# Performance work log

Measured on AMD Instinct MI355X. Metric: run time of the kernel, lower is better.

## Reference

```python
import jax, jax.numpy as jnp
import numpy as np

N_NODES = 100000
EPS = 1e-5


def _layernorm(h, gamma, beta):
    mu = jnp.mean(h, axis=-1, keepdims=True)
    var = jnp.mean(jnp.square(h - mu), axis=-1, keepdims=True)
    return (h - mu) * jax.lax.rsqrt(var + EPS) * gamma + beta


def _gcn_conv(x, W, b, row, col, inv_sqrt_deg):
    # PyG GCNConv: y = D^{-1/2} (A + I) D^{-1/2} (x W) + b, self-loops already in row/col
    xw = x @ W                                  # [N, C]
    norm = inv_sqrt_deg[row] * inv_sqrt_deg[col]  # [E+N]
    msg = xw[row] * norm[:, None]               # [E+N, C] gather
    agg = jax.ops.segment_sum(msg, col, num_segments=N_NODES)  # scatter-add
    return agg + b


def setup_inputs() -> dict:
    key = jax.random.key(0)
    ks = jax.random.split(key, 8)
    C = 256
    x = jax.random.normal(ks[0], (N_NODES, C), dtype=jnp.float32)
    all_edges = jax.random.randint(ks[1], (2, 1600000), 0, N_NODES, dtype=jnp.int32)
    s = 1.0 / np.sqrt(C)
    W1 = jax.random.uniform(ks[2], (C, C), jnp.float32, -s, s)
    b1 = jnp.zeros((C,), jnp.float32)
    W2 = jax.random.uniform(ks[3], (C, C), jnp.float32, -s, s)
    b2 = jnp.zeros((C,), jnp.float32)
    gamma = jnp.ones((C,), jnp.float32)
    beta = jnp.zeros((C,), jnp.float32)
    return {"x": x, "all_edges": all_edges, "W1": W1, "b1": b1,
            "W2": W2, "b2": b2, "gamma": gamma, "beta": beta}


def reference(x, all_edges, W1, b1, W2, b2, gamma, beta):
    # add self-loops
    loops = jnp.arange(N_NODES, dtype=all_edges.dtype)
    row = jnp.concatenate([all_edges[0], loops])
    col = jnp.concatenate([all_edges[1], loops])
    deg = jax.ops.segment_sum(jnp.ones_like(col, dtype=x.dtype), col,
                              num_segments=N_NODES)
    inv_sqrt_deg = jnp.where(deg > 0, jax.lax.rsqrt(deg), 0.0)

    z1 = jax.nn.relu(_layernorm(_gcn_conv(x, W1, b1, row, col, inv_sqrt_deg), gamma, beta))
    z2 = jax.nn.relu(_layernorm(_gcn_conv(z1, W2, b2, row, col, inv_sqrt_deg), gamma, beta))
    return (z1, z2)
```

## Files before the change

kernel.cpp:

```cpp
#include <hip/hip_runtime.h>
#include <cstdint>

#define C_DIM 256
#define EPS 1e-5f

typedef __attribute__((ext_vector_type(8))) short short8;
typedef __attribute__((ext_vector_type(4))) float f32x4;

__device__ __forceinline__ ushort f2bf(float f) {
  uint32_t u = __float_as_uint(f);
  u = (u + 0x7fffu + ((u >> 16) & 1u)) >> 16;
  return (ushort)u;
}
__device__ __forceinline__ float bflo(uint32_t p) { return __uint_as_float(p << 16); }
__device__ __forceinline__ float bfhi(uint32_t p) { return __uint_as_float(p & 0xffff0000u); }

__global__ void k_count(const int* __restrict__ col, int E, int* cnt) {
  int e = blockIdx.x * blockDim.x + threadIdx.x;
  if (e < E) atomicAdd(&cnt[col[e]], 1);
}

__global__ void k_isd(int* cnt, float* isd, int n) {
  int i = blockIdx.x * blockDim.x + threadIdx.x;
  if (i < n) { isd[i] = rsqrtf((float)(cnt[i] + 1)); cnt[i] = 0; }
}

__global__ void k_scan1(const int* __restrict__ cnt, int* excl, int* bsum, int n) {
  __shared__ int s[1024];
  int i = blockIdx.x * 1024 + threadIdx.x;
  int v = (i < n) ? cnt[i] : 0;
  s[threadIdx.x] = v;
  __syncthreads();
  for (int off = 1; off < 1024; off <<= 1) {
    int t = (threadIdx.x >= off) ? s[threadIdx.x - off] : 0;
    __syncthreads();
    s[threadIdx.x] += t;
    __syncthreads();
  }
  if (i < n) excl[i] = s[threadIdx.x] - v;
  if (threadIdx.x == 1023) bsum[blockIdx.x] = s[1023];
}

__global__ void k_scan2(int* bsum, int nb) {
  __shared__ int s[1024];
  int v = (threadIdx.x < nb) ? bsum[threadIdx.x] : 0;
  s[threadIdx.x] = v;
  __syncthreads();
  for (int off = 1; off < 1024; off <<= 1) {
    int t = (threadIdx.x >= off) ? s[threadIdx.x - off] : 0;
    __syncthreads();
    s[threadIdx.x] += t;
    __syncthreads();
  }
  if (threadIdx.x < nb) bsum[threadIdx.x] = s[threadIdx.x] - v;
}

__global__ void k_scan3(int* excl, const int* __restrict__ bsum, int n, int E) {
  int i = blockIdx.x * 1024 + threadIdx.x;
  if (i < n) excl[i] += bsum[blockIdx.x];
  if (i == 0) excl[n] = E;
}

__global__ void k_fill(const int* __restrict__ row, const int* __restrict__ col, int E,
                       const int* __restrict__ row_ptr, int* cursor,
                       const float* __restrict__ isd, int2* __restrict__ edat) {
  int e = blockIdx.x * blockDim.x + threadIdx.x;
  if (e < E) {
    int d = col[e], s = row[e];
    int p = row_ptr[d] + atomicAdd(&cursor[d], 1);
    edat[p] = make_int2(s, __float_as_int(isd[s] * isd[d]));
  }
}

__global__ void k_cvt_x(const float* __restrict__ x, ushort* __restrict__ xb, int n4) {
  int i = blockIdx.x * blockDim.x + threadIdx.x;
  if (i < n4) {
    float4 v = ((const float4*)x)[i];
    ushort4 o;
    o.x = f2bf(v.x); o.y = f2bf(v.y); o.z = f2bf(v.z); o.w = f2bf(v.w);
    ((ushort4*)xb)[i] = o;
  }
}

__global__ void k_cvt_w(const float* __restrict__ W1, const float* __restrict__ W2,
                        ushort* __restrict__ Wt1, ushort* __restrict__ Wt2) {
  int i = blockIdx.x * blockDim.x + threadIdx.x;
  int n = i >> 8, k = i & 255;
  Wt1[i] = f2bf(W1[k * 256 + n]);
  Wt2[i] = f2bf(W2[k * 256 + n]);
}

__global__ __launch_bounds__(256) void k_gemm_bf16(const ushort* __restrict__ A,
                                                   const ushort* __restrict__ Wt,
                                                   ushort* __restrict__ Cb, int M) {
  __shared__ ushort As[128 * 64];
  __shared__ ushort Bs[128 * 64];
  const int tid = threadIdx.x;
  const int wave = tid >> 6, lane = tid & 63;
  const int bm = blockIdx.x * 128;
  const int bn = blockIdx.y * 128;
  const int wm = (wave >> 1) * 64, wn = (wave & 1) * 64;

  f32x4 acc[4][4] = {};

  const int r_off = lane >> 3;
  const int cc = lane & 7;

  for (int k0 = 0; k0 < C_DIM; k0 += 64) {
#pragma unroll
    for (int j = 0; j < 4; j++) {
      int rl = wave * 32 + j * 8 + r_off;
      int c = cc ^ (rl & 7);
      int gm = bm + rl; if (gm >= M) gm = M - 1;
      const ushort* ga = &A[(size_t)gm * C_DIM + k0 + c * 8];
      ushort* la = &As[(size_t)(wave * 32 + j * 8) * 64];
      __builtin_amdgcn_global_load_lds((const __attribute__((address_space(1))) void*)ga,
                                       (__attribute__((address_space(3))) void*)la, 16, 0, 0);
      const ushort* gb = &Wt[(size_t)(bn + rl) * C_DIM + k0 + c * 8];
      ushort* lb = &Bs[(size_t)(wave * 32 + j * 8) * 64];
      __builtin_amdgcn_global_load_lds((const __attribute__((address_space(1))) void*)gb,
                                       (__attribute__((address_space(3))) void*)lb, 16, 0, 0);
    }
    __syncthreads();
#pragma unroll
    for (int s = 0; s < 2; s++) {
      short8 af[4], bfr[4];
#pragma unroll
      for (int t = 0; t < 4; t++) {
        int ra = wm + t * 16 + (lane & 15);
        int ca = s * 4 + (lane >> 4);
        af[t] = *(const short8*)&As[ra * 64 + ((ca ^ (ra & 7)) << 3)];
        int rb = wn + t * 16 + (lane & 15);
        bfr[t] = *(const short8*)&Bs[rb * 64 + ((ca ^ (rb & 7)) << 3)];
      }
#pragma unroll
      for (int mt = 0; mt < 4; mt++)
#pragma unroll
        for (int nt = 0; nt < 4; nt++)
          acc[mt][nt] = __builtin_amdgcn_mfma_f32_16x16x32_bf16(af[mt], bfr[nt], acc[mt][nt], 0, 0, 0);
    }
    __syncthreads();
  }

#pragma unroll
  for (int mt = 0; mt < 4; mt++) {
#pragma unroll
    for (int nt = 0; nt < 4; nt++) {
      int col = bn + wn + nt * 16 + (lane & 15);
      int row0 = bm + wm + mt * 16 + ((lane >> 4) << 2);
#pragma unroll
      for (int r = 0; r < 4; r++) {
        int row = row0 + r;
        if (row < M) Cb[(size_t)row * C_DIM + col] = f2bf(acc[mt][nt][r]);
      }
    }
  }
}

__global__ __launch_bounds__(256) void k_agg_ln(const ushort* __restrict__ xwb,
    const int2* __restrict__ edat, const int* __restrict__ row_ptr,
    const float* __restrict__ isd,
    const float* __restrict__ bias, const float* __restrict__ gamma,
    const float* __restrict__ beta, float* __restrict__ out,
    ushort* __restrict__ outb, int n) {
  int i = blockIdx.x * 4 + (threadIdx.x >> 6);
  int lane = threadIdx.x & 63;
  if (i >= n) return;
  const uint2* xw2 = (const uint2*)xwb;

  float si = isd[i];
  float sn = si * si;
  uint2 p = xw2[(size_t)i * 64 + lane];
  float a0 = bflo(p.x) * sn, a1 = bfhi(p.x) * sn;
  float a2 = bflo(p.y) * sn, a3 = bfhi(p.y) * sn;

  int e0 = row_ptr[i], e1 = row_ptr[i + 1];
  int e = e0;
  for (; e + 7 < e1; e += 8) {
    int2 ed0 = edat[e],     ed1 = edat[e + 1], ed2 = edat[e + 2], ed3 = edat[e + 3];
    int2 ed4 = edat[e + 4], ed5 = edat[e + 5], ed6 = edat[e + 6], ed7 = edat[e + 7];
    uint2 v0 = xw2[(size_t)ed0.x * 64 + lane];
    uint2 v1 = xw2[(size_t)ed1.x * 64 + lane];
    uint2 v2 = xw2[(size_t)ed2.x * 64 + lane];
    uint2 v3 = xw2[(size_t)ed3.x * 64 + lane];
    uint2 v4 = xw2[(size_t)ed4.x * 64 + lane];
    uint2 v5 = xw2[(size_t)ed5.x * 64 + lane];
    uint2 v6 = xw2[(size_t)ed6.x * 64 + lane];
    uint2 v7 = xw2[(size_t)ed7.x * 64 + lane];
    float w0 = __int_as_float(ed0.y), w1 = __int_as_float(ed1.y);
    float w2 = __int_as_float(ed2.y), w3 = __int_as_float(ed3.y);
    float w4 = __int_as_float(ed4.y), w5 = __int_as_float(ed5.y);
    float w6 = __int_as_float(ed6.y), w7 = __int_as_float(ed7.y);
    a0 += bflo(v0.x) * w0 + bflo(v1.x) * w1 + bflo(v2.x) * w2 + bflo(v3.x) * w3
        + bflo(v4.x) * w4 + bflo(v5.x) * w5 + bflo(v6.x) * w6 + bflo(v7.x) * w7;
    a1 += bfhi(v0.x) * w0 + bfhi(v1.x) * w1 + bfhi(v2.x) * w2 + bfhi(v3.x) * w3
        + bfhi(v4.x) * w4 + bfhi(v5.x) * w5 + bfhi(v6.x) * w6 + bfhi(v7.x) * w7;
    a2 += bflo(v0.y) * w0 + bflo(v1.y) * w1 + bflo(v2.y) * w2 + bflo(v3.y) * w3
        + bflo(v4.y) * w4 + bflo(v5.y) * w5 + bflo(v6.y) * w6 + bflo(v7.y) * w7;
    a3 += bfhi(v0.y) * w0 + bfhi(v1.y) * w1 + bfhi(v2.y) * w2 + bfhi(v3.y) * w3
        + bfhi(v4.y) * w4 + bfhi(v5.y) * w5 + bfhi(v6.y) * w6 + bfhi(v7.y) * w7;
  }
  for (; e + 3 < e1; e += 4) {
    int2 ed0 = edat[e], ed1 = edat[e + 1], ed2 = edat[e + 2], ed3 = edat[e + 3];
    uint2 v0 = xw2[(size_t)ed0.x * 64 + lane];
    uint2 v1 = xw2[(size_t)ed1.x * 64 + lane];
    uint2 v2 = xw2[(size_t)ed2.x * 64 + lane];
    uint2 v3 = xw2[(size_t)ed3.x * 64 + lane];
    float w0 = __int_as_float(ed0.y), w1 = __int_as_float(ed1.y);
    float w2 = __int_as_float(ed2.y), w3 = __int_as_float(ed3.y);
    a0 += bflo(v0.x) * w0 + bflo(v1.x) * w1 + bflo(v2.x) * w2 + bflo(v3.x) * w3;
    a1 += bfhi(v0.x) * w0 + bfhi(v1.x) * w1 + bfhi(v2.x) * w2 + bfhi(v3.x) * w3;
    a2 += bflo(v0.y) * w0 + bflo(v1.y) * w1 + bflo(v2.y) * w2 + bflo(v3.y) * w3;
    a3 += bfhi(v0.y) * w0 + bfhi(v1.y) * w1 + bfhi(v2.y) * w2 + bfhi(v3.y) * w3;
  }
  for (; e < e1; e++) {
    int2 ed = edat[e];
    float w0 = __int_as_float(ed.y);
    uint2 v0 = xw2[(size_t)ed.x * 64 + lane];
    a0 += bflo(v0.x) * w0; a1 += bfhi(v0.x) * w0;
    a2 += bflo(v0.y) * w0; a3 += bfhi(v0.y) * w0;
  }

  float4 bv = ((const float4*)bias)[lane];
  a0 += bv.x; a1 += bv.y; a2 += bv.z; a3 += bv.w;

  float sum = a0 + a1 + a2 + a3;
  float sq = a0 * a0 + a1 * a1 + a2 * a2 + a3 * a3;
#pragma unroll
  for (int off = 32; off >= 1; off >>= 1) {
    sum += __shfl_xor(sum, off, 64);
    sq += __shfl_xor(sq, off, 64);
  }
  float mu = sum * (1.0f / C_DIM);
  float var = sq * (1.0f / C_DIM) - mu * mu;
  float rs = rsqrtf(var + EPS);

  float4 g = ((const float4*)gamma)[lane];
  float4 bt = ((const float4*)beta)[lane];
  f32x4 o;
  o[0] = fmaxf((a0 - mu) * rs * g.x + bt.x, 0.0f);
  o[1] = fmaxf((a1 - mu) * rs * g.y + bt.y, 0.0f);
  o[2] = fmaxf((a2 - mu) * rs * g.z + bt.z, 0.0f);
  o[3] = fmaxf((a3 - mu) * rs * g.w + bt.w, 0.0f);
  __builtin_nontemporal_store(o, (f32x4*)&out[((size_t)i * 64 + lane) * 4]);

  if (outb) {
    uint2 q;
    q.x = (uint32_t)f2bf(o[0]) | ((uint32_t)f2bf(o[1]) << 16);
    q.y = (uint32_t)f2bf(o[2]) | ((uint32_t)f2bf(o[3]) << 16);
    ((uint2*)outb)[(size_t)i * 64 + lane] = q;
  }
}

extern "C" void kernel_launch(void* const* d_in, const int* in_sizes, int n_in,
                              void* d_out, int out_size, void* d_ws, size_t ws_size,
                              hipStream_t stream) {
  const float* x = (const float*)d_in[0];
  const int* edges = (const int*)d_in[1];
  const float* W1 = (const float*)d_in[2];
  const float* b1 = (const float*)d_in[3];
  const float* W2 = (const float*)d_in[4];
  const float* b2 = (const float*)d_in[5];
  const float* gamma = (const float*)d_in[6];
  const float* beta = (const float*)d_in[7];

  int N = in_sizes[0] / C_DIM;
  int E = in_sizes[1] / 2;
  const int* row = edges;
  const int* col = edges + E;

  char* ws = (char*)d_ws;
  size_t off = 0;
  auto alloc = [&](size_t bytes) -> void* {
    void* p = ws + off;
    off = (off + bytes + 255) & ~(size_t)255;
    return p;
  };
  ushort* xwb = (ushort*)alloc((size_t)N * C_DIM * 2);
  ushort* xb  = (ushort*)alloc((size_t)N * C_DIM * 2);
  ushort* Wt1 = (ushort*)alloc(65536 * 2);
  ushort* Wt2 = (ushort*)alloc(65536 * 2);
  int* cnt = (int*)alloc((size_t)N * 4);
  float* isd = (float*)alloc((size_t)N * 4);
  int* row_ptr = (int*)alloc((size_t)(N + 1) * 4);
  int nb = (N + 1023) / 1024;
  int* bsum = (int*)alloc((size_t)nb * 4);
  int2* edat = (int2*)alloc((size_t)E * 8);

  float* z1 = (float*)d_out;
  float* z2 = (float*)d_out + (size_t)N * C_DIM;

  int n4 = N * C_DIM / 4;
  k_cvt_x<<<(n4 + 255) / 256, 256, 0, stream>>>(x, xb, n4);
  k_cvt_w<<<256, 256, 0, stream>>>(W1, W2, Wt1, Wt2);

  (void)hipMemsetAsync(cnt, 0, (size_t)N * 4, stream);
  k_count<<<(E + 255) / 256, 256, 0, stream>>>(col, E, cnt);
  k_scan1<<<nb, 1024, 0, stream>>>(cnt, row_ptr, bsum, N);
  k_scan2<<<1, 1024, 0, stream>>>(bsum, nb);
  k_scan3<<<nb, 1024, 0, stream>>>(row_ptr, bsum, N, E);
  k_isd<<<(N + 255) / 256, 256, 0, stream>>>(cnt, isd, N);
  k_fill<<<(E + 255) / 256, 256, 0, stream>>>(row, col, E, row_ptr, cnt, isd, edat);

  dim3 ggrid((N + 127) / 128, 2);
  int agg_blocks = (N + 3) / 4;

  k_gemm_bf16<<<ggrid, 256, 0, stream>>>(xb, Wt1, xwb, N);
  k_agg_ln<<<agg_blocks, 256, 0, stream>>>(xwb, edat, row_ptr, isd, b1, gamma, beta, z1, xb, N);
  k_gemm_bf16<<<ggrid, 256, 0, stream>>>(xb, Wt2, xwb, N);
  k_agg_ln<<<agg_blocks, 256, 0, stream>>>(xwb, edat, row_ptr, isd, b2, gamma, beta, z2, nullptr, N);
}
```

Baseline: 730.7 us.

## Restructure bf16 GEMM to keep full-K weight tile in LDS and stream A from global

The GEMM now loads the whole 128x256 weight slice into LDS once per block, with an XOR swizzle. A fragments are read straight from global memory into registers, with no LDS staging. Each wave computes a 64x128 output tile, and the block tile grows to 256 rows, which halves the grid in M. This drops the per-K-step barriers and A's LDS round trip, but it raises register pressure (32 accumulators) and uses 64KB of LDS, which can lower occupancy. Global A loads are also not shared across the waves.

Result: no change. 739.5 us (+1.2%).

```diff
diff --git a/kernel.cpp b/kernel.cpp
--- a/kernel.cpp
+++ b/kernel.cpp
@@ -93,60 +93,56 @@
 __global__ __launch_bounds__(256) void k_gemm_bf16(const ushort* __restrict__ A,
                                                    const ushort* __restrict__ Wt,
                                                    ushort* __restrict__ Cb, int M) {
-  __shared__ ushort As[128 * 64];
-  __shared__ ushort Bs[128 * 64];
+  __shared__ ushort Bs[128 * 256];
   const int tid = threadIdx.x;
   const int wave = tid >> 6, lane = tid & 63;
-  const int bm = blockIdx.x * 128;
+  const int bm = blockIdx.x * 256;
   const int bn = blockIdx.y * 128;
-  const int wm = (wave >> 1) * 64, wn = (wave & 1) * 64;
-
-  f32x4 acc[4][4] = {};
-
-  const int r_off = lane >> 3;
-  const int cc = lane & 7;
-
-  for (int k0 = 0; k0 < C_DIM; k0 += 64) {
-#pragma unroll
-    for (int j = 0; j < 4; j++) {
-      int rl = wave * 32 + j * 8 + r_off;
-      int c = cc ^ (rl & 7);
-      int gm = bm + rl; if (gm >= M) gm = M - 1;
-      const ushort* ga = &A[(size_t)gm * C_DIM + k0 + c * 8];
-      ushort* la = &As[(size_t)(wave * 32 + j * 8) * 64];
-      __builtin_amdgcn_global_load_lds((const __attribute__((address_space(1))) void*)ga,
-                                       (__attribute__((address_space(3))) void*)la, 16, 0, 0);
-      const ushort* gb = &Wt[(size_t)(bn + rl) * C_DIM + k0 + c * 8];
-      ushort* lb = &Bs[(size_t)(wave * 32 + j * 8) * 64];
-      __builtin_amdgcn_global_load_lds((const __attribute__((address_space(1))) void*)gb,
-                                       (__attribute__((address_space(3))) void*)lb, 16, 0, 0);
+  const int wm = wave * 64;
+
+#pragma unroll
+  for (int j = 0; j < 16; j++) {
+    int r0 = wave * 32 + j * 2;
+    int r = r0 + (lane >> 5);
+    int csrc = (lane & 31) ^ (r & 7);
+    const ushort* gb = &Wt[(size_t)(bn + r) * C_DIM + csrc * 8];
+    ushort* lb = &Bs[r0 * 256];
+    __builtin_amdgcn_global_load_lds((const __attribute__((address_space(1))) void*)gb,
+                                     (__attribute__((address_space(3))) void*)lb, 16, 0, 0);
+  }
+  __syncthreads();
+
+  f32x4 acc[4][8] = {};
+  const int arow = bm + wm + (lane & 15);
+  const int koff = (lane >> 4) * 8;
+
+#pragma unroll
+  for (int ks = 0; ks < 8; ks++) {
+    short8 af[4];
+#pragma unroll
+    for (int mt = 0; mt < 4; mt++) {
+      int g = arow + mt * 16; if (g >= M) g = M - 1;
+      af[mt] = *(const short8*)&A[(size_t)g * C_DIM + ks * 32 + koff];
     }
-    __syncthreads();
-#pragma unroll
-    for (int s = 0; s < 2; s++) {
-      short8 af[4], bfr[4];
-#pragma unroll
-      for (int t = 0; t < 4; t++) {
-        int ra = wm + t * 16 + (lane & 15);
-        int ca = s * 4 + (lane >> 4);
-        af[t] = *(const short8*)&As[ra * 64 + ((ca ^ (ra & 7)) << 3)];
-        int rb = wn + t * 16 + (lane & 15);
-        bfr[t] = *(const short8*)&Bs[rb * 64 + ((ca ^ (rb & 7)) << 3)];
-      }
-#pragma unroll
-      for (int mt = 0; mt < 4; mt++)
-#pragma unroll
-        for (int nt = 0; nt < 4; nt++)
-          acc[mt][nt] = __builtin_amdgcn_mfma_f32_16x16x32_bf16(af[mt], bfr[nt], acc[mt][nt], 0, 0, 0);
+    short8 bfr[8];
+    int cl = ks * 4 + (lane >> 4);
+#pragma unroll
+    for (int nt = 0; nt < 8; nt++) {
+      int rb = nt * 16 + (lane & 15);
+      bfr[nt] = *(const short8*)&Bs[rb * 256 + ((cl ^ (rb & 7)) << 3)];
     }
-    __syncthreads();
+#pragma unroll
+    for (int mt = 0; mt < 4; mt++)
+#pragma unroll
+      for (int nt = 0; nt < 8; nt++)
+        acc[mt][nt] = __builtin_amdgcn_mfma_f32_16x16x32_bf16(af[mt], bfr[nt], acc[mt][nt], 0, 0, 0);
   }
 
 #pragma unroll
   for (int mt = 0; mt < 4; mt++) {
 #pragma unroll
-    for (int nt = 0; nt < 4; nt++) {
-      int col = bn + wn + nt * 16 + (lane & 15);
+    for (int nt = 0; nt < 8; nt++) {
+      int col = bn + nt * 16 + (lane & 15);
       int row0 = bm + wm + mt * 16 + ((lane >> 4) << 2);
 #pragma unroll
       for (int r = 0; r < 4; r++) {
@@ -302,7 +298,7 @@
   k_isd<<<(N + 255) / 256, 256, 0, stream>>>(cnt, isd, N);
   k_fill<<<(E + 255) / 256, 256, 0, stream>>>(row, col, E, row_ptr, cnt, isd, edat);
 
-  dim3 ggrid((N + 127) / 128, 2);
+  dim3 ggrid((N + 255) / 256, 2);
   int agg_blocks = (N + 3) / 4;
 
   k_gemm_bf16<<<ggrid, 256, 0, stream>>>(xb, Wt1, xwb, N);
```
